# Kernel optimization log

Hardware: AMD Instinct MI355X
Metric: run time of the kernel (lower is better)

The kernel has to match this reference:

```python
import jax, jax.numpy as jnp
import numpy as np

B, L, S, H, E, D = 2, 2048, 2048, 8, 64, 64

def setup_inputs() -> dict:
    key = jax.random.key(0)
    kq, kk, kv = jax.random.split(key, 3)
    queries = jax.random.normal(kq, (B, L, H, E), dtype=jnp.float32)
    keys = jax.random.normal(kk, (B, S, H, E), dtype=jnp.float32)
    values = jax.random.normal(kv, (B, S, H, D), dtype=jnp.float32)
    return {"queries": queries, "keys": keys, "values": values}

def reference(queries, keys, values):
    # queries: [B,L,H,E], keys: [B,S,H,E], values: [B,S,H,D]
    E_ = queries.shape[-1]
    scale = 1.0 / jnp.sqrt(jnp.asarray(E_, dtype=queries.dtype))
    # scores: [B,H,L,S]
    scores = jnp.einsum('blhe,bshe->bhls', queries, keys)
    # mask_flag=False, use_relative_pos=False, dropout=0.0 -> identity
    A = jax.nn.softmax(scale * scores, axis=-1)
    # output: [B,L,H,D]
    V = jnp.einsum('bhls,bshd->blhd', A, values)
    return V
```

## Files before the change

### kernel.cpp

```cpp
#include <hip/hip_runtime.h>
#include <hip/hip_bf16.h>


#define LOG2E 1.44269504088896340736f

#if __has_builtin(__builtin_amdgcn_exp2f)
#define EXP2(x) __builtin_amdgcn_exp2f(x)
#else
#define EXP2(x) exp2f(x)
#endif

typedef __attribute__((ext_vector_type(8))) short bf16x8;
typedef __attribute__((ext_vector_type(4))) float f32x4;
typedef __attribute__((ext_vector_type(16))) float f32x16;

static constexpr int Bc = 2, Lc = 2048, Sc = 2048, Hc = 8, Ec = 64, Dc = 64;
static constexpr int BH = Bc * Hc;
static constexpr int ELEMS = Bc * Lc * Hc * Ec;

static __device__ __forceinline__ unsigned short bfb(float x) {
  union { __hip_bfloat16 h; unsigned short u; } c;
  c.h = __float2bfloat16(x);
  return c.u;
}

__global__ __launch_bounds__(256) void cvt_q_kernel(const float* __restrict__ Q,
                                                    __hip_bfloat16* __restrict__ Qc) {
  int t = blockIdx.x * 256 + threadIdx.x;
  int f = t * 4;
  int e = f & 63;
  int h = (f >> 6) & 7;
  int l = (f >> 9) & 2047;
  int b = f >> 20;
  float4 v = *reinterpret_cast<const float4*>(Q + f);
  int o = (((b << 3) + h) * Lc + l) * 64 + e;
  ushort4 w;
  w.x = bfb(v.x * 0.125f);
  w.y = bfb(v.y * 0.125f);
  w.z = bfb(v.z * 0.125f);
  w.w = bfb(v.w * 0.125f);
  *reinterpret_cast<ushort4*>(Qc + o) = w;
}

__global__ __launch_bounds__(256) void cvt_k_kernel(const float* __restrict__ K,
                                                    __hip_bfloat16* __restrict__ Kc) {
  int t = blockIdx.x * 256 + threadIdx.x;
  int f = t * 8;
  int e = f & 63;
  int h = (f >> 6) & 7;
  int s = (f >> 9) & 2047;
  int b = f >> 20;
  float4 v0 = *reinterpret_cast<const float4*>(K + f);
  float4 v1 = *reinterpret_cast<const float4*>(K + f + 4);
  int es = e >> 4, hi = (e >> 3) & 1;
  int kb = s >> 5, qi = s & 31;
  int o = ((b << 3) + h) * (Sc * 64) + kb * 2048 + es * 512 + hi * 256 + qi * 8;
  union { ushort u[8]; uint4 q; } pk;
  pk.u[0] = bfb(v0.x); pk.u[1] = bfb(v0.y); pk.u[2] = bfb(v0.z); pk.u[3] = bfb(v0.w);
  pk.u[4] = bfb(v1.x); pk.u[5] = bfb(v1.y); pk.u[6] = bfb(v1.z); pk.u[7] = bfb(v1.w);
  *reinterpret_cast<uint4*>(Kc + o) = pk.q;
}

__global__ __launch_bounds__(64) void cvt_v_kernel(const float* __restrict__ V,
                                                   __hip_bfloat16* __restrict__ Vt) {
  __shared__ __hip_bfloat16 tile[64][68];
  const int s0 = blockIdx.x * 64;
  const int bh = blockIdx.y;
  const int b = bh >> 3, h = bh & 7;
  const int lane = threadIdx.x;
#pragma unroll 4
  for (int j = 0; j < 64; ++j) {
    float v = V[((b * Sc + s0 + j) * Hc + h) * 64 + lane];
    tile[j][lane] = __float2bfloat16(v);
  }
  __syncthreads();
  const int qi = lane & 31, hi = lane >> 5;
  __hip_bfloat16* Vb = Vt + bh * (Sc * 64);
#pragma unroll
  for (int kb2 = 0; kb2 < 2; ++kb2)
#pragma unroll
    for (int d0 = 0; d0 < 2; ++d0)
#pragma unroll
      for (int ks = 0; ks < 2; ++ks) {
        union { ushort u[8]; uint4 q; } pk;
#pragma unroll
        for (int j = 0; j < 8; ++j) {
          union { __hip_bfloat16 h; ushort u; } c;
          c.h = tile[kb2 * 32 + ks * 16 + hi * 8 + j][d0 * 32 + qi];
          pk.u[j] = c.u;
        }
        int o = ((s0 >> 5) + kb2) * 2048 + d0 * 1024 + ks * 512 + lane * 8;
        *reinterpret_cast<uint4*>(Vb + o) = pk.q;
      }
}

static __device__ __forceinline__ void plswap(unsigned a, unsigned b,
                                              unsigned& o0, unsigned& o1, int hi) {
#if __has_builtin(__builtin_amdgcn_permlane32_swap)
  auto r = __builtin_amdgcn_permlane32_swap(a, b, false, false);
  o0 = r[0];
  o1 = r[1];
#else
  unsigned ax = (unsigned)__shfl_xor((int)a, 32);
  unsigned bx = (unsigned)__shfl_xor((int)b, 32);
  o0 = hi ? bx : a;
  o1 = hi ? b : ax;
#endif
}

static __device__ __forceinline__ unsigned pkbf(float a, float b) {
  union { __hip_bfloat162 h; unsigned u; } c;
  c.h = __float22bfloat162_rn(make_float2(a, b));
  return c.u;
}

static __device__ __forceinline__ bf16x8 pack4(unsigned w0, unsigned w1,
                                               unsigned w2, unsigned w3) {
  union { unsigned u[4]; bf16x8 v; } c;
  c.u[0] = w0; c.u[1] = w1; c.u[2] = w2; c.u[3] = w3;
  return c.v;
}

__global__ __launch_bounds__(256, 4) void attn_kernel(const __hip_bfloat16* __restrict__ Qc,
                                                      const __hip_bfloat16* __restrict__ Kc,
                                                      const __hip_bfloat16* __restrict__ Vt,
                                                      float* __restrict__ Out) {
  __shared__ float obuf[4][2][16][64];
  __shared__ float mlb[4][2][32];

  const int lid = blockIdx.x;
  const int xcd = lid & 7;
  const int i = lid >> 3;
  const int bh = (xcd << 1) | (i >> 6);
  const int q0 = (i & 63) << 5;
  const int w = threadIdx.x >> 6;
  const int lane = threadIdx.x & 63;
  const int qi = lane & 31;
  const int hi = lane >> 5;

  const __hip_bfloat16* Qh = Qc + (bh * Lc + q0) * Ec;
  const __hip_bfloat16* Kh = Kc + bh * (Sc * 64);
  const __hip_bfloat16* Vh = Vt + bh * (Sc * 64);

  bf16x8 qf0 = *reinterpret_cast<const bf16x8*>(Qh + qi * 64 + 0 * 16 + hi * 8);
  bf16x8 qf1 = *reinterpret_cast<const bf16x8*>(Qh + qi * 64 + 1 * 16 + hi * 8);
  bf16x8 qf2 = *reinterpret_cast<const bf16x8*>(Qh + qi * 64 + 2 * 16 + hi * 8);
  bf16x8 qf3 = *reinterpret_cast<const bf16x8*>(Qh + qi * 64 + 3 * 16 + hi * 8);

  f32x16 oa, ob;
#pragma unroll
  for (int r = 0; r < 16; ++r) { oa[r] = 0.f; ob[r] = 0.f; }
  float m = -1.0e30f, l = 0.f;

  for (int s = w * 32; s < Sc; s += 128) {
    const __hip_bfloat16* Kp = Kh + (s >> 5) * 2048 + lane * 8;
    bf16x8 k0 = *reinterpret_cast<const bf16x8*>(Kp + 0 * 512);
    bf16x8 k1 = *reinterpret_cast<const bf16x8*>(Kp + 1 * 512);
    bf16x8 k2 = *reinterpret_cast<const bf16x8*>(Kp + 2 * 512);
    bf16x8 k3 = *reinterpret_cast<const bf16x8*>(Kp + 3 * 512);
    const __hip_bfloat16* Vp = Vh + (s >> 5) * 2048 + lane * 8;
    bf16x8 v00 = *reinterpret_cast<const bf16x8*>(Vp + 0 * 512);
    bf16x8 v01 = *reinterpret_cast<const bf16x8*>(Vp + 1 * 512);
    bf16x8 v10 = *reinterpret_cast<const bf16x8*>(Vp + 2 * 512);
    bf16x8 v11 = *reinterpret_cast<const bf16x8*>(Vp + 3 * 512);

    f32x16 sc;
#pragma unroll
    for (int r = 0; r < 16; ++r) sc[r] = 0.f;
    __builtin_amdgcn_s_setprio(1);
    sc = __builtin_amdgcn_mfma_f32_32x32x16_bf16(k0, qf0, sc, 0, 0, 0);
    sc = __builtin_amdgcn_mfma_f32_32x32x16_bf16(k1, qf1, sc, 0, 0, 0);
    sc = __builtin_amdgcn_mfma_f32_32x32x16_bf16(k2, qf2, sc, 0, 0, 0);
    sc = __builtin_amdgcn_mfma_f32_32x32x16_bf16(k3, qf3, sc, 0, 0, 0);
    __builtin_amdgcn_s_setprio(0);

    float x0 = fmaxf(fmaxf(sc[0], sc[1]), fmaxf(sc[2], sc[3]));
    float x1 = fmaxf(fmaxf(sc[4], sc[5]), fmaxf(sc[6], sc[7]));
    float x2 = fmaxf(fmaxf(sc[8], sc[9]), fmaxf(sc[10], sc[11]));
    float x3 = fmaxf(fmaxf(sc[12], sc[13]), fmaxf(sc[14], sc[15]));
    float mx = fmaxf(fmaxf(x0, x1), fmaxf(x2, x3));
    unsigned ua, ub;
    plswap(__float_as_uint(mx), __float_as_uint(mx), ua, ub, hi);
    mx = fmaxf(__uint_as_float(ua), __uint_as_float(ub));

    if (__any(mx > m + 8.0f)) {
      float mnew = fmaxf(m, mx);
      float corr = EXP2((m - mnew) * LOG2E);
      l *= corr;
#pragma unroll
      for (int r = 0; r < 16; ++r) { oa[r] *= corr; ob[r] *= corr; }
      m = mnew;
    }

#pragma unroll
    for (int r = 0; r < 16; ++r) sc[r] = EXP2((sc[r] - m) * LOG2E);

    float r0 = (sc[0] + sc[1]) + (sc[2] + sc[3]);
    float r1 = (sc[4] + sc[5]) + (sc[6] + sc[7]);
    float r2 = (sc[8] + sc[9]) + (sc[10] + sc[11]);
    float r3 = (sc[12] + sc[13]) + (sc[14] + sc[15]);
    float rs = (r0 + r1) + (r2 + r3);
    plswap(__float_as_uint(rs), __float_as_uint(rs), ua, ub, hi);
    rs = __uint_as_float(ua) + __uint_as_float(ub);
    l += rs;

    unsigned c0, c1, c2, c3, w0, w1, w2, w3;
    c0 = pkbf(sc[0], sc[1]);  c1 = pkbf(sc[4], sc[5]);
    c2 = pkbf(sc[2], sc[3]);  c3 = pkbf(sc[6], sc[7]);
    plswap(c0, c1, w0, w2, hi);
    plswap(c2, c3, w1, w3, hi);
    bf16x8 pb0 = pack4(w0, w1, w2, w3);
    c0 = pkbf(sc[8], sc[9]);   c1 = pkbf(sc[12], sc[13]);
    c2 = pkbf(sc[10], sc[11]); c3 = pkbf(sc[14], sc[15]);
    plswap(c0, c1, w0, w2, hi);
    plswap(c2, c3, w1, w3, hi);
    bf16x8 pb1 = pack4(w0, w1, w2, w3);

    __builtin_amdgcn_s_setprio(1);
    oa = __builtin_amdgcn_mfma_f32_32x32x16_bf16(v00, pb0, oa, 0, 0, 0);
    oa = __builtin_amdgcn_mfma_f32_32x32x16_bf16(v01, pb1, oa, 0, 0, 0);
    ob = __builtin_amdgcn_mfma_f32_32x32x16_bf16(v10, pb0, ob, 0, 0, 0);
    ob = __builtin_amdgcn_mfma_f32_32x32x16_bf16(v11, pb1, ob, 0, 0, 0);
    __builtin_amdgcn_s_setprio(0);
  }

  if (hi == 0) { mlb[w][0][qi] = m; mlb[w][1][qi] = l; }
  __syncthreads();
  float mm = fmaxf(fmaxf(mlb[0][0][qi], mlb[1][0][qi]),
                   fmaxf(mlb[2][0][qi], mlb[3][0][qi]));
  float Lt = 0.f;
#pragma unroll
  for (int sw = 0; sw < 4; ++sw)
    Lt += EXP2((mlb[sw][0][qi] - mm) * LOG2E) * mlb[sw][1][qi];
  float myf = EXP2((m - mm) * LOG2E);
  float inv = 1.0f / Lt;
#pragma unroll
  for (int r = 0; r < 16; ++r) {
    obuf[w][0][r][lane] = oa[r] * myf;
    obuf[w][1][r][lane] = ob[r] * myf;
  }
  __syncthreads();
  const int d0 = w >> 1, rr = (w & 1) * 8;
  const int b = bh >> 3, h = bh & 7;
  float* orow = Out + ((b * Lc + q0 + qi) * Hc + h) * Dc;
#pragma unroll
  for (int t = 0; t < 2; ++t) {
    f32x4 acc;
#pragma unroll
    for (int j = 0; j < 4; ++j) {
      const int r = rr + 4 * t + j;
      acc[j] = (obuf[0][d0][r][lane] + obuf[1][d0][r][lane] +
                obuf[2][d0][r][lane] + obuf[3][d0][r][lane]) * inv;
    }
    const int dbase = d0 * 32 + ((rr + 4 * t) >> 2) * 8 + hi * 4;
    *reinterpret_cast<f32x4*>(orow + dbase) = acc;
  }
}

extern "C" void kernel_launch(void* const* d_in, const int* in_sizes, int n_in,
                              void* d_out, int out_size, void* d_ws, size_t ws_size,
                              hipStream_t stream) {
  const float* Q = (const float*)d_in[0];
  const float* K = (const float*)d_in[1];
  const float* V = (const float*)d_in[2];
  float* out = (float*)d_out;

  __hip_bfloat16* Qc = (__hip_bfloat16*)d_ws;
  __hip_bfloat16* Kc = Qc + ELEMS;
  __hip_bfloat16* Vt = Kc + ELEMS;

  cvt_q_kernel<<<(ELEMS / 4) / 256, 256, 0, stream>>>(Q, Qc);
  cvt_k_kernel<<<(ELEMS / 8) / 256, 256, 0, stream>>>(K, Kc);
  cvt_v_kernel<<<dim3(Sc / 64, BH), 64, 0, stream>>>(V, Vt);
  attn_kernel<<<dim3(1024), 256, 0, stream>>>(Qc, Kc, Vt, out);
}
```

Baseline: 49.91 us.

## Process two query groups per block, fuse Q conversion, merge K/V prep kernels

The attention kernel now handles 64 query rows per block (two 32-row groups), so each K/V fragment loaded is reused for twice the MFMA work, and the grid halves to 512 blocks. Q is read as fp32 and converted to bf16 inside the attention kernel, which removes the separate Q conversion pass. The 1/sqrt(E) scale is folded into the exp2 constant, and the rescale threshold widens to match the unscaled scores. The K and V conversions are merged into one launch, cutting launch count from four to two, at the cost of more registers per thread (launch bounds lowered to 2 waves) and fewer blocks for latency hiding.

```diff
diff --git a/kernel.cpp b/kernel.cpp
--- a/kernel.cpp
+++ b/kernel.cpp
@@ -3,6 +3,7 @@
 
 
 #define LOG2E 1.44269504088896340736f
+#define SCL2 0.18033688011112042f
 
 #if __has_builtin(__builtin_amdgcn_exp2f)
 #define EXP2(x) __builtin_amdgcn_exp2f(x)
@@ -23,75 +24,16 @@
   c.h = __float2bfloat16(x);
   return c.u;
 }
-
-__global__ __launch_bounds__(256) void cvt_q_kernel(const float* __restrict__ Q,
-                                                    __hip_bfloat16* __restrict__ Qc) {
-  int t = blockIdx.x * 256 + threadIdx.x;
-  int f = t * 4;
-  int e = f & 63;
-  int h = (f >> 6) & 7;
-  int l = (f >> 9) & 2047;
-  int b = f >> 20;
-  float4 v = *reinterpret_cast<const float4*>(Q + f);
-  int o = (((b << 3) + h) * Lc + l) * 64 + e;
-  ushort4 w;
-  w.x = bfb(v.x * 0.125f);
-  w.y = bfb(v.y * 0.125f);
-  w.z = bfb(v.z * 0.125f);
-  w.w = bfb(v.w * 0.125f);
-  *reinterpret_cast<ushort4*>(Qc + o) = w;
-}
-
-__global__ __launch_bounds__(256) void cvt_k_kernel(const float* __restrict__ K,
-                                                    __hip_bfloat16* __restrict__ Kc) {
-  int t = blockIdx.x * 256 + threadIdx.x;
-  int f = t * 8;
-  int e = f & 63;
-  int h = (f >> 6) & 7;
-  int s = (f >> 9) & 2047;
-  int b = f >> 20;
-  float4 v0 = *reinterpret_cast<const float4*>(K + f);
-  float4 v1 = *reinterpret_cast<const float4*>(K + f + 4);
-  int es = e >> 4, hi = (e >> 3) & 1;
-  int kb = s >> 5, qi = s & 31;
-  int o = ((b << 3) + h) * (Sc * 64) + kb * 2048 + es * 512 + hi * 256 + qi * 8;
-  union { ushort u[8]; uint4 q; } pk;
-  pk.u[0] = bfb(v0.x); pk.u[1] = bfb(v0.y); pk.u[2] = bfb(v0.z); pk.u[3] = bfb(v0.w);
-  pk.u[4] = bfb(v1.x); pk.u[5] = bfb(v1.y); pk.u[6] = bfb(v1.z); pk.u[7] = bfb(v1.w);
-  *reinterpret_cast<uint4*>(Kc + o) = pk.q;
-}
-
-__global__ __launch_bounds__(64) void cvt_v_kernel(const float* __restrict__ V,
-                                                   __hip_bfloat16* __restrict__ Vt) {
-  __shared__ __hip_bfloat16 tile[64][68];
-  const int s0 = blockIdx.x * 64;
-  const int bh = blockIdx.y;
-  const int b = bh >> 3, h = bh & 7;
-  const int lane = threadIdx.x;
-#pragma unroll 4
-  for (int j = 0; j < 64; ++j) {
-    float v = V[((b * Sc + s0 + j) * Hc + h) * 64 + lane];
-    tile[j][lane] = __float2bfloat16(v);
-  }
-  __syncthreads();
-  const int qi = lane & 31, hi = lane >> 5;
-  __hip_bfloat16* Vb = Vt + bh * (Sc * 64);
-#pragma unroll
-  for (int kb2 = 0; kb2 < 2; ++kb2)
-#pragma unroll
-    for (int d0 = 0; d0 < 2; ++d0)
-#pragma unroll
-      for (int ks = 0; ks < 2; ++ks) {
-        union { ushort u[8]; uint4 q; } pk;
-#pragma unroll
-        for (int j = 0; j < 8; ++j) {
-          union { __hip_bfloat16 h; ushort u; } c;
-          c.h = tile[kb2 * 32 + ks * 16 + hi * 8 + j][d0 * 32 + qi];
-          pk.u[j] = c.u;
-        }
-        int o = ((s0 >> 5) + kb2) * 2048 + d0 * 1024 + ks * 512 + lane * 8;
-        *reinterpret_cast<uint4*>(Vb + o) = pk.q;
-      }
+static __device__ __forceinline__ unsigned pkbf(float a, float b) {
+  union { __hip_bfloat162 h; unsigned u; } c;
+  c.h = __float22bfloat162_rn(make_float2(a, b));
+  return c.u;
+}
+static __device__ __forceinline__ bf16x8 pack4(unsigned w0, unsigned w1,
+                                               unsigned w2, unsigned w3) {
+  union { unsigned u[4]; bf16x8 v; } c;
+  c.u[0] = w0; c.u[1] = w1; c.u[2] = w2; c.u[3] = w3;
+  return c.v;
 }
 
 static __device__ __forceinline__ void plswap(unsigned a, unsigned b,
@@ -108,49 +50,145 @@
 #endif
 }
 
-static __device__ __forceinline__ unsigned pkbf(float a, float b) {
-  union { __hip_bfloat162 h; unsigned u; } c;
-  c.h = __float22bfloat162_rn(make_float2(a, b));
-  return c.u;
-}
-
-static __device__ __forceinline__ bf16x8 pack4(unsigned w0, unsigned w1,
-                                               unsigned w2, unsigned w3) {
-  union { unsigned u[4]; bf16x8 v; } c;
-  c.u[0] = w0; c.u[1] = w1; c.u[2] = w2; c.u[3] = w3;
-  return c.v;
-}
-
-__global__ __launch_bounds__(256, 4) void attn_kernel(const __hip_bfloat16* __restrict__ Qc,
+__global__ __launch_bounds__(256) void prep_kv_kernel(const float* __restrict__ K,
+                                                      const float* __restrict__ V,
+                                                      __hip_bfloat16* __restrict__ Kc,
+                                                      __hip_bfloat16* __restrict__ Vt) {
+  __shared__ __hip_bfloat16 tile[4][64][68];
+  if (blockIdx.x < 1024) {
+    int t = blockIdx.x * 256 + threadIdx.x;
+    int f = t * 8;
+    int e = f & 63;
+    int h = (f >> 6) & 7;
+    int s = (f >> 9) & 2047;
+    int b = f >> 20;
+    float4 v0 = *reinterpret_cast<const float4*>(K + f);
+    float4 v1 = *reinterpret_cast<const float4*>(K + f + 4);
+    int es = e >> 4, hi = (e >> 3) & 1;
+    int kb = s >> 5, qi = s & 31;
+    int o = ((b << 3) + h) * (Sc * 64) + kb * 2048 + es * 512 + hi * 256 + qi * 8;
+    union { ushort u[8]; uint4 q; } pk;
+    pk.u[0] = bfb(v0.x); pk.u[1] = bfb(v0.y); pk.u[2] = bfb(v0.z); pk.u[3] = bfb(v0.w);
+    pk.u[4] = bfb(v1.x); pk.u[5] = bfb(v1.y); pk.u[6] = bfb(v1.z); pk.u[7] = bfb(v1.w);
+    *reinterpret_cast<uint4*>(Kc + o) = pk.q;
+  } else {
+    const int w = threadIdx.x >> 6;
+    const int lane = threadIdx.x & 63;
+    const int task = (blockIdx.x - 1024) * 4 + w;
+    const int st = task & 31;
+    const int bh = task >> 5;
+    const int s0 = st * 64;
+    const int b = bh >> 3, h = bh & 7;
+#pragma unroll 4
+    for (int j = 0; j < 64; ++j) {
+      float v = V[((b * Sc + s0 + j) * Hc + h) * 64 + lane];
+      tile[w][j][lane] = __float2bfloat16(v);
+    }
+    __syncthreads();
+    const int qi = lane & 31, hi = lane >> 5;
+    __hip_bfloat16* Vb = Vt + bh * (Sc * 64);
+#pragma unroll
+    for (int kb2 = 0; kb2 < 2; ++kb2)
+#pragma unroll
+      for (int d0 = 0; d0 < 2; ++d0)
+#pragma unroll
+        for (int ks = 0; ks < 2; ++ks) {
+          union { ushort u[8]; uint4 q; } pk;
+#pragma unroll
+          for (int j = 0; j < 8; ++j) {
+            union { __hip_bfloat16 h; ushort u; } c;
+            c.h = tile[w][kb2 * 32 + ks * 16 + hi * 8 + j][d0 * 32 + qi];
+            pk.u[j] = c.u;
+          }
+          int o = ((s0 >> 5) + kb2) * 2048 + d0 * 1024 + ks * 512 + lane * 8;
+          *reinterpret_cast<uint4*>(Vb + o) = pk.q;
+        }
+  }
+}
+
+static __device__ __forceinline__ void sm_group(f32x16& sc, float& m, float& l,
+                                                f32x16& oA, f32x16& oB, int hi,
+                                                bf16x8& pb0, bf16x8& pb1) {
+  float x0 = fmaxf(fmaxf(sc[0], sc[1]), fmaxf(sc[2], sc[3]));
+  float x1 = fmaxf(fmaxf(sc[4], sc[5]), fmaxf(sc[6], sc[7]));
+  float x2 = fmaxf(fmaxf(sc[8], sc[9]), fmaxf(sc[10], sc[11]));
+  float x3 = fmaxf(fmaxf(sc[12], sc[13]), fmaxf(sc[14], sc[15]));
+  float mx = fmaxf(fmaxf(x0, x1), fmaxf(x2, x3));
+  unsigned ua, ub;
+  plswap(__float_as_uint(mx), __float_as_uint(mx), ua, ub, hi);
+  mx = fmaxf(__uint_as_float(ua), __uint_as_float(ub));
+
+  if (__any(mx > m + 64.0f)) {
+    float mnew = fmaxf(m, mx);
+    float corr = EXP2((m - mnew) * SCL2);
+    l *= corr;
+#pragma unroll
+    for (int r = 0; r < 16; ++r) { oA[r] *= corr; oB[r] *= corr; }
+    m = mnew;
+  }
+  float mL = m * SCL2;
+#pragma unroll
+  for (int r = 0; r < 16; ++r) sc[r] = EXP2(sc[r] * SCL2 - mL);
+
+  float r0 = (sc[0] + sc[1]) + (sc[2] + sc[3]);
+  float r1 = (sc[4] + sc[5]) + (sc[6] + sc[7]);
+  float r2 = (sc[8] + sc[9]) + (sc[10] + sc[11]);
+  float r3 = (sc[12] + sc[13]) + (sc[14] + sc[15]);
+  float rs = (r0 + r1) + (r2 + r3);
+  plswap(__float_as_uint(rs), __float_as_uint(rs), ua, ub, hi);
+  rs = __uint_as_float(ua) + __uint_as_float(ub);
+  l += rs;
+
+  unsigned c0, c1, c2, c3, y0, y1, y2, y3;
+  c0 = pkbf(sc[0], sc[1]);  c1 = pkbf(sc[4], sc[5]);
+  c2 = pkbf(sc[2], sc[3]);  c3 = pkbf(sc[6], sc[7]);
+  plswap(c0, c1, y0, y2, hi);
+  plswap(c2, c3, y1, y3, hi);
+  pb0 = pack4(y0, y1, y2, y3);
+  c0 = pkbf(sc[8], sc[9]);   c1 = pkbf(sc[12], sc[13]);
+  c2 = pkbf(sc[10], sc[11]); c3 = pkbf(sc[14], sc[15]);
+  plswap(c0, c1, y0, y2, hi);
+  plswap(c2, c3, y1, y3, hi);
+  pb1 = pack4(y0, y1, y2, y3);
+}
+
+__global__ __launch_bounds__(256, 2) void attn_kernel(const float* __restrict__ Qf,
                                                       const __hip_bfloat16* __restrict__ Kc,
                                                       const __hip_bfloat16* __restrict__ Vt,
                                                       float* __restrict__ Out) {
   __shared__ float obuf[4][2][16][64];
-  __shared__ float mlb[4][2][32];
+  __shared__ float mlb[2][4][2][32];
 
   const int lid = blockIdx.x;
   const int xcd = lid & 7;
   const int i = lid >> 3;
-  const int bh = (xcd << 1) | (i >> 6);
-  const int q0 = (i & 63) << 5;
+  const int bh = (xcd << 1) | (i >> 5);
+  const int q0 = (i & 31) << 6;
   const int w = threadIdx.x >> 6;
   const int lane = threadIdx.x & 63;
   const int qi = lane & 31;
   const int hi = lane >> 5;
-
-  const __hip_bfloat16* Qh = Qc + (bh * Lc + q0) * Ec;
+  const int b = bh >> 3, h = bh & 7;
+
   const __hip_bfloat16* Kh = Kc + bh * (Sc * 64);
   const __hip_bfloat16* Vh = Vt + bh * (Sc * 64);
 
-  bf16x8 qf0 = *reinterpret_cast<const bf16x8*>(Qh + qi * 64 + 0 * 16 + hi * 8);
-  bf16x8 qf1 = *reinterpret_cast<const bf16x8*>(Qh + qi * 64 + 1 * 16 + hi * 8);
-  bf16x8 qf2 = *reinterpret_cast<const bf16x8*>(Qh + qi * 64 + 2 * 16 + hi * 8);
-  bf16x8 qf3 = *reinterpret_cast<const bf16x8*>(Qh + qi * 64 + 3 * 16 + hi * 8);
-
-  f32x16 oa, ob;
-#pragma unroll
-  for (int r = 0; r < 16; ++r) { oa[r] = 0.f; ob[r] = 0.f; }
-  float m = -1.0e30f, l = 0.f;
+  bf16x8 qf[2][4];
+#pragma unroll
+  for (int g = 0; g < 2; ++g) {
+    const float* qrow = Qf + ((b * Lc + q0 + g * 32 + qi) * Hc + h) * 64 + hi * 8;
+#pragma unroll
+    for (int es = 0; es < 4; ++es) {
+      float4 a = *reinterpret_cast<const float4*>(qrow + es * 16);
+      float4 c = *reinterpret_cast<const float4*>(qrow + es * 16 + 4);
+      qf[g][es] = pack4(pkbf(a.x, a.y), pkbf(a.z, a.w), pkbf(c.x, c.y), pkbf(c.z, c.w));
+    }
+  }
+
+  f32x16 oa0, ob0, oa1, ob1;
+#pragma unroll
+  for (int r = 0; r < 16; ++r) { oa0[r] = 0.f; ob0[r] = 0.f; oa1[r] = 0.f; ob1[r] = 0.f; }
+  float m0 = -1.0e30f, l0 = 0.f, m1 = -1.0e30f, l1 = 0.f;
 
   for (int s = w * 32; s < Sc; s += 128) {
     const __hip_bfloat16* Kp = Kh + (s >> 5) * 2048 + lane * 8;
@@ -164,96 +202,81 @@
     bf16x8 v10 = *reinterpret_cast<const bf16x8*>(Vp + 2 * 512);
     bf16x8 v11 = *reinterpret_cast<const bf16x8*>(Vp + 3 * 512);
 
-    f32x16 sc;
-#pragma unroll
-    for (int r = 0; r < 16; ++r) sc[r] = 0.f;
+    f32x16 sc0, sc1;
+#pragma unroll
+    for (int r = 0; r < 16; ++r) { sc0[r] = 0.f; sc1[r] = 0.f; }
     __builtin_amdgcn_s_setprio(1);
-    sc = __builtin_amdgcn_mfma_f32_32x32x16_bf16(k0, qf0, sc, 0, 0, 0);
-    sc = __builtin_amdgcn_mfma_f32_32x32x16_bf16(k1, qf1, sc, 0, 0, 0);
-    sc = __builtin_amdgcn_mfma_f32_32x32x16_bf16(k2, qf2, sc, 0, 0, 0);
-    sc = __builtin_amdgcn_mfma_f32_32x32x16_bf16(k3, qf3, sc, 0, 0, 0);
+    sc0 = __builtin_amdgcn_mfma_f32_32x32x16_bf16(k0, qf[0][0], sc0, 0, 0, 0);
+    sc0 = __builtin_amdgcn_mfma_f32_32x32x16_bf16(k1, qf[0][1], sc0, 0, 0, 0);
+    sc0 = __builtin_amdgcn_mfma_f32_32x32x16_bf16(k2, qf[0][2], sc0, 0, 0, 0);
+    sc0 = __builtin_amdgcn_mfma_f32_32x32x16_bf16(k3, qf[0][3], sc0, 0, 0, 0);
+    sc1 = __builtin_amdgcn_mfma_f32_32x32x16_bf16(k0, qf[1][0], sc1, 0, 0, 0);
+    sc1 = __builtin_amdgcn_mfma_f32_32x32x16_bf16(k1, qf[1][1], sc1, 0, 0, 0);
+    sc1 = __builtin_amdgcn_mfma_f32_32x32x16_bf16(k2, qf[1][2], sc1, 0, 0, 0);
+    sc1 = __builtin_amdgcn_mfma_f32_32x32x16_bf16(k3, qf[1][3], sc1, 0, 0, 0);
     __builtin_amdgcn_s_setprio(0);
 
-    float x0 = fmaxf(fmaxf(sc[0], sc[1]), fmaxf(sc[2], sc[3]));
-    float x1 = fmaxf(fmaxf(sc[4], sc[5]), fmaxf(sc[6], sc[7]));
-    float x2 = fmaxf(fmaxf(sc[8], sc[9]), fmaxf(sc[10], sc[11]));
-    float x3 = fmaxf(fmaxf(sc[12], sc[13]), fmaxf(sc[14], sc[15]));
-    float mx = fmaxf(fmaxf(x0, x1), fmaxf(x2, x3));
-    unsigned ua, ub;
-    plswap(__float_as_uint(mx), __float_as_uint(mx), ua, ub, hi);
-    mx = fmaxf(__uint_as_float(ua), __uint_as_float(ub));
-
-    if (__any(mx > m + 8.0f)) {
-      float mnew = fmaxf(m, mx);
-      float corr = EXP2((m - mnew) * LOG2E);
-      l *= corr;
-#pragma unroll
-      for (int r = 0; r < 16; ++r) { oa[r] *= corr; ob[r] *= corr; }
-      m = mnew;
-    }
-
-#pragma unroll
-    for (int r = 0; r < 16; ++r) sc[r] = EXP2((sc[r] - m) * LOG2E);
-
-    float r0 = (sc[0] + sc[1]) + (sc[2] + sc[3]);
-    float r1 = (sc[4] + sc[5]) + (sc[6] + sc[7]);
-    float r2 = (sc[8] + sc[9]) + (sc[10] + sc[11]);
-    float r3 = (sc[12] + sc[13]) + (sc[14] + sc[15]);
-    float rs = (r0 + r1) + (r2 + r3);
-    plswap(__float_as_uint(rs), __float_as_uint(rs), ua, ub, hi);
-    rs = __uint_as_float(ua) + __uint_as_float(ub);
-    l += rs;
-
-    unsigned c0, c1, c2, c3, w0, w1, w2, w3;
-    c0 = pkbf(sc[0], sc[1]);  c1 = pkbf(sc[4], sc[5]);
-    c2 = pkbf(sc[2], sc[3]);  c3 = pkbf(sc[6], sc[7]);
-    plswap(c0, c1, w0, w2, hi);
-    plswap(c2, c3, w1, w3, hi);
-    bf16x8 pb0 = pack4(w0, w1, w2, w3);
-    c0 = pkbf(sc[8], sc[9]);   c1 = pkbf(sc[12], sc[13]);
-    c2 = pkbf(sc[10], sc[11]); c3 = pkbf(sc[14], sc[15]);
-    plswap(c0, c1, w0, w2, hi);
-    plswap(c2, c3, w1, w3, hi);
-    bf16x8 pb1 = pack4(w0, w1, w2, w3);
-
+    bf16x8 pb0, pb1;
+    sm_group(sc0, m0, l0, oa0, ob0, hi, pb0, pb1);
     __builtin_amdgcn_s_setprio(1);
-    oa = __builtin_amdgcn_mfma_f32_32x32x16_bf16(v00, pb0, oa, 0, 0, 0);
-    oa = __builtin_amdgcn_mfma_f32_32x32x16_bf16(v01, pb1, oa, 0, 0, 0);
-    ob = __builtin_amdgcn_mfma_f32_32x32x16_bf16(v10, pb0, ob, 0, 0, 0);
-    ob = __builtin_amdgcn_mfma_f32_32x32x16_bf16(v11, pb1, ob, 0, 0, 0);
+    oa0 = __builtin_amdgcn_mfma_f32_32x32x16_bf16(v00, pb0, oa0, 0, 0, 0);
+    oa0 = __builtin_amdgcn_mfma_f32_32x32x16_bf16(v01, pb1, oa0, 0, 0, 0);
+    ob0 = __builtin_amdgcn_mfma_f32_32x32x16_bf16(v10, pb0, ob0, 0, 0, 0);
+    ob0 = __builtin_amdgcn_mfma_f32_32x32x16_bf16(v11, pb1, ob0, 0, 0, 0);
     __builtin_amdgcn_s_setprio(0);
-  }
-
-  if (hi == 0) { mlb[w][0][qi] = m; mlb[w][1][qi] = l; }
+
+    sm_group(sc1, m1, l1, oa1, ob1, hi, pb0, pb1);
+    __builtin_amdgcn_s_setprio(1);
+    oa1 = __builtin_amdgcn_mfma_f32_32x32x16_bf16(v00, pb0, oa1, 0, 0, 0);
+    oa1 = __builtin_amdgcn_mfma_f32_32x32x16_bf16(v01, pb1, oa1, 0, 0, 0);
+    ob1 = __builtin_amdgcn_mfma_f32_32x32x16_bf16(v10, pb0, ob1, 0, 0, 0);
+    ob1 = __builtin_amdgcn_mfma_f32_32x32x16_bf16(v11, pb1, ob1, 0, 0, 0);
+    __builtin_amdgcn_s_setprio(0);
+  }
+
+  if (hi == 0) {
+    mlb[0][w][0][qi] = m0; mlb[0][w][1][qi] = l0;
+    mlb[1][w][0][qi] = m1; mlb[1][w][1][qi] = l1;
+  }
   __syncthreads();
-  float mm = fmaxf(fmaxf(mlb[0][0][qi], mlb[1][0][qi]),
-                   fmaxf(mlb[2][0][qi], mlb[3][0][qi]));
-  float Lt = 0.f;
-#pragma unroll
-  for (int sw = 0; sw < 4; ++sw)
-    Lt += EXP2((mlb[sw][0][qi] - mm) * LOG2E) * mlb[sw][1][qi];
-  float myf = EXP2((m - mm) * LOG2E);
-  float inv = 1.0f / Lt;
-#pragma unroll
-  for (int r = 0; r < 16; ++r) {
-    obuf[w][0][r][lane] = oa[r] * myf;
-    obuf[w][1][r][lane] = ob[r] * myf;
-  }
-  __syncthreads();
+  float myf[2], inv[2];
+#pragma unroll
+  for (int g = 0; g < 2; ++g) {
+    float mm = fmaxf(fmaxf(mlb[g][0][0][qi], mlb[g][1][0][qi]),
+                     fmaxf(mlb[g][2][0][qi], mlb[g][3][0][qi]));
+    float Lt = 0.f;
+#pragma unroll
+    for (int sw = 0; sw < 4; ++sw)
+      Lt += EXP2((mlb[g][sw][0][qi] - mm) * SCL2) * mlb[g][sw][1][qi];
+    float mreg = g ? m1 : m0;
+    myf[g] = EXP2((mreg - mm) * SCL2);
+    inv[g] = 1.0f / Lt;
+  }
   const int d0 = w >> 1, rr = (w & 1) * 8;
-  const int b = bh >> 3, h = bh & 7;
-  float* orow = Out + ((b * Lc + q0 + qi) * Hc + h) * Dc;
-#pragma unroll
-  for (int t = 0; t < 2; ++t) {
-    f32x4 acc;
-#pragma unroll
-    for (int j = 0; j < 4; ++j) {
-      const int r = rr + 4 * t + j;
-      acc[j] = (obuf[0][d0][r][lane] + obuf[1][d0][r][lane] +
-                obuf[2][d0][r][lane] + obuf[3][d0][r][lane]) * inv;
-    }
-    const int dbase = d0 * 32 + ((rr + 4 * t) >> 2) * 8 + hi * 4;
-    *reinterpret_cast<f32x4*>(orow + dbase) = acc;
+#pragma unroll
+  for (int g = 0; g < 2; ++g) {
+    if (g) __syncthreads();
+    const f32x16& A = g ? oa1 : oa0;
+    const f32x16& Bv = g ? ob1 : ob0;
+#pragma unroll
+    for (int r = 0; r < 16; ++r) {
+      obuf[w][0][r][lane] = A[r] * myf[g];
+      obuf[w][1][r][lane] = Bv[r] * myf[g];
+    }
+    __syncthreads();
+    float* orow = Out + ((b * Lc + q0 + g * 32 + qi) * Hc + h) * Dc;
+#pragma unroll
+    for (int t = 0; t < 2; ++t) {
+      f32x4 acc;
+#pragma unroll
+      for (int j = 0; j < 4; ++j) {
+        const int r = rr + 4 * t + j;
+        acc[j] = (obuf[0][d0][r][lane] + obuf[1][d0][r][lane] +
+                  obuf[2][d0][r][lane] + obuf[3][d0][r][lane]) * inv[g];
+      }
+      const int dbase = d0 * 32 + ((rr + 4 * t) >> 2) * 8 + hi * 4;
+      *reinterpret_cast<f32x4*>(orow + dbase) = acc;
+    }
   }
 }
 
@@ -265,12 +288,9 @@
   const float* V = (const float*)d_in[2];
   float* out = (float*)d_out;
 
-  __hip_bfloat16* Qc = (__hip_bfloat16*)d_ws;
-  __hip_bfloat16* Kc = Qc + ELEMS;
+  __hip_bfloat16* Kc = (__hip_bfloat16*)d_ws;
   __hip_bfloat16* Vt = Kc + ELEMS;
 
-  cvt_q_kernel<<<(ELEMS / 4) / 256, 256, 0, stream>>>(Q, Qc);
-  cvt_k_kernel<<<(ELEMS / 8) / 256, 256, 0, stream>>>(K, Kc);
-  cvt_v_kernel<<<dim3(Sc / 64, BH), 64, 0, stream>>>(V, Vt);
-  attn_kernel<<<dim3(1024), 256, 0, stream>>>(Qc, Kc, Vt, out);
-}
+  prep_kv_kernel<<<dim3(1152), 256, 0, stream>>>(K, V, Kc, Vt);
+  attn_kernel<<<dim3(512), 256, 0, stream>>>(Q, Kc, Vt, out);
+}
```

After: 46.38 us. 7.1% less time.
